# Kernel tuning notes

Measured on AMD Instinct MI355X. Metric: run time of the kernel, lower is better.

The kernel has to match this reference:

```python
import jax, jax.numpy as jnp
import numpy as np

EMBED_DIM = 1024
NUM_HEADS = 16
FFN_DIM = 4096
N_QUBITS = 8
LN_EPS = 1e-5


def _layernorm(x, g, b):
    mu = jnp.mean(x, axis=-1, keepdims=True)
    var = jnp.mean(jnp.square(x - mu), axis=-1, keepdims=True)
    return (x - mu) * jax.lax.rsqrt(var + LN_EPS) * g + b


def setup_inputs() -> dict:
    key = jax.random.key(0)
    ks = jax.random.split(key, 12)
    E, F_, Q = EMBED_DIM, FFN_DIM, N_QUBITS
    s = 1.0 / np.sqrt(E)
    return {
        "x": jax.random.normal(ks[0], (4, 2048, E), dtype=jnp.float32),
        "wq": jax.random.normal(ks[1], (E, E), dtype=jnp.float32) * s,
        "wk": jax.random.normal(ks[2], (E, E), dtype=jnp.float32) * s,
        "wv": jax.random.normal(ks[3], (E, E), dtype=jnp.float32) * s,
        "wo": jax.random.normal(ks[4], (E, E), dtype=jnp.float32) * s,
        "theta": jax.random.normal(ks[5], (Q,), dtype=jnp.float32),
        "w1": jax.random.normal(ks[6], (Q, F_), dtype=jnp.float32) * (1.0 / np.sqrt(Q)),
        "w2": jax.random.normal(ks[7], (F_, E), dtype=jnp.float32) * (1.0 / np.sqrt(F_)),
        "ln1_g": jnp.ones((E,), dtype=jnp.float32),
        "ln1_b": jnp.zeros((E,), dtype=jnp.float32),
        "ln2_g": jnp.ones((E,), dtype=jnp.float32),
        "ln2_b": jnp.zeros((E,), dtype=jnp.float32),
    }


def reference(x, wq, wk, wv, wo, theta, w1, w2, ln1_g, ln1_b, ln2_g, ln2_b):
    B, S, E = x.shape
    H, Dk = NUM_HEADS, E // NUM_HEADS
    # ---- multi-head attention ----
    q = (x @ wq).reshape(B, S, H, Dk).transpose(0, 2, 1, 3)  # [B,H,S,Dk]
    k = (x @ wk).reshape(B, S, H, Dk).transpose(0, 2, 1, 3)
    v = (x @ wv).reshape(B, S, H, Dk).transpose(0, 2, 1, 3)
    scores = jnp.einsum("bhsd,bhtd->bhst", q, k) / np.sqrt(Dk)
    attn = jax.nn.softmax(scores, axis=-1)
    ctx = jnp.einsum("bhst,bhtd->bhsd", attn, v)
    ctx = ctx.transpose(0, 2, 1, 3).reshape(B, S, E)
    attn_out = ctx @ wo
    x1 = _layernorm(x + attn_out, ln1_g, ln1_b)
    # ---- quantum FFN ----
    # Per qubit w: |0> -> RX(x1_w) -> RX(x1_w) -> RX(theta_w); <Z> = cos(2*x1_w + theta_w)
    q_out = jnp.cos(2.0 * x1[..., :N_QUBITS] + theta)  # [B,S,Q]
    ffn_out = jax.nn.relu(q_out @ w1) @ w2  # [B,S,E]
    return _layernorm(x1 + ffn_out, ln2_g, ln2_b)
```

## Files before the change

kernel.cpp:

```cpp
#include <hip/hip_runtime.h>
#include <hip/hip_bf16.h>


typedef __attribute__((ext_vector_type(8))) short bf16x8;
typedef __attribute__((ext_vector_type(16))) float f32x16;
typedef __attribute__((ext_vector_type(4))) unsigned short u16x4;

__device__ __forceinline__ unsigned short f2bf(float f) {
  union { float f; unsigned int u; } v; v.f = f;
  return (unsigned short)((v.u + 0x7FFFu + ((v.u >> 16) & 1u)) >> 16);
}
__device__ __forceinline__ float bf2f(unsigned short h) {
  union { unsigned int u; float f; } v; v.u = ((unsigned int)h) << 16;
  return v.f;
}
__device__ __forceinline__ f32x16 mfma32(bf16x8 a, bf16x8 b, f32x16 c) {
  return __builtin_amdgcn_mfma_f32_32x32x16_bf16(a, b, c, 0, 0, 0);
}
__device__ __forceinline__ void lds_cp16(const void* g, void* l) {
  __builtin_amdgcn_global_load_lds(
      (const __attribute__((address_space(1))) unsigned int*)g,
      (__attribute__((address_space(3))) unsigned int*)l, 16, 0, 0);
}

#define QG_CONV(P, FC0, FC1)                                                  \
  {                                                                           \
    int x0a, x0b, x1a, x1b, x2a, x2b, x3a, x3b;                               \
    asm("v_cvt_pk_bf16_f32 %0, %1, %2" : "=v"(x0a) : "v"(P[0]),  "v"(P[1]));  \
    asm("v_cvt_pk_bf16_f32 %0, %1, %2" : "=v"(x0b) : "v"(P[2]),  "v"(P[3]));  \
    asm("v_cvt_pk_bf16_f32 %0, %1, %2" : "=v"(x1a) : "v"(P[4]),  "v"(P[5]));  \
    asm("v_cvt_pk_bf16_f32 %0, %1, %2" : "=v"(x1b) : "v"(P[6]),  "v"(P[7]));  \
    asm("v_cvt_pk_bf16_f32 %0, %1, %2" : "=v"(x2a) : "v"(P[8]),  "v"(P[9]));  \
    asm("v_cvt_pk_bf16_f32 %0, %1, %2" : "=v"(x2b) : "v"(P[10]), "v"(P[11])); \
    asm("v_cvt_pk_bf16_f32 %0, %1, %2" : "=v"(x3a) : "v"(P[12]), "v"(P[13])); \
    asm("v_cvt_pk_bf16_f32 %0, %1, %2" : "=v"(x3b) : "v"(P[14]), "v"(P[15])); \
    asm("v_permlane32_swap_b32 %0, %1" : "+v"(x0a), "+v"(x1a));               \
    asm("v_permlane32_swap_b32 %0, %1" : "+v"(x0b), "+v"(x1b));               \
    asm("v_permlane32_swap_b32 %0, %1" : "+v"(x2a), "+v"(x3a));               \
    asm("v_permlane32_swap_b32 %0, %1" : "+v"(x2b), "+v"(x3b));               \
    union { int u[4]; bf16x8 v; } f0_, f1_;                                   \
    f0_.u[0] = x0a; f0_.u[1] = x0b; f0_.u[2] = x1a; f0_.u[3] = x1b;           \
    f1_.u[0] = x2a; f1_.u[1] = x2b; f1_.u[2] = x3a; f1_.u[3] = x3b;           \
    FC0 = f0_.v; FC1 = f1_.v;                                                 \
  }

__global__ __launch_bounds__(256) void cast_x_kernel(const float* __restrict__ in,
                                                     unsigned short* __restrict__ out,
                                                     int n4) {
  int i = blockIdx.x * 256 + threadIdx.x;
  if (i >= n4) return;
  float4 v = ((const float4*)in)[i];
  u16x4 o = { f2bf(v.x), f2bf(v.y), f2bf(v.z), f2bf(v.w) };
  ((u16x4*)out)[i] = o;
}

__global__ __launch_bounds__(256) void transpose_cast_kernel(const float* __restrict__ in,
                                                             unsigned short* __restrict__ out,
                                                             int K, int N) {
  __shared__ float tile[32][33];
  const int n0 = blockIdx.x * 32, k0 = blockIdx.y * 32;
  const int tx = threadIdx.x, ty = threadIdx.y;
#pragma unroll
  for (int i = 0; i < 32; i += 8)
    tile[ty + i][tx] = in[(long)(k0 + ty + i) * N + n0 + tx];
  __syncthreads();
#pragma unroll
  for (int i = 0; i < 32; i += 8)
    out[(long)(n0 + ty + i) * K + k0 + tx] = f2bf(tile[tx][ty + i]);
}

__global__ __launch_bounds__(256) void w1t_kernel(const float* __restrict__ w1,
                                                  unsigned short* __restrict__ w1t) {
  const int f = blockIdx.x * 256 + threadIdx.x;
  unsigned short v[8];
#pragma unroll
  for (int q = 0; q < 8; q++) v[q] = f2bf(w1[q * 4096 + f]);
  *(u16x4*)(w1t + f * 8)     = (u16x4){v[0], v[1], v[2], v[3]};
  *(u16x4*)(w1t + f * 8 + 4) = (u16x4){v[4], v[5], v[6], v[7]};
}

__global__ __launch_bounds__(256) void vt_kernel(const unsigned short* __restrict__ qkv,
                                                 unsigned short* __restrict__ vT) {
  __shared__ unsigned short tile[32][34];
  const int t0 = blockIdx.x * 32, d0 = blockIdx.y * 32, bh = blockIdx.z;
  const int b = bh >> 4, h = bh & 15;
  const int tx = threadIdx.x, ty = threadIdx.y;
  const unsigned short* src = qkv + (long)(b * 2048 + t0) * 3072 + 2048 + h * 64 + d0;
#pragma unroll
  for (int i = 0; i < 32; i += 8)
    tile[ty + i][tx] = src[(long)(ty + i) * 3072 + tx];
  __syncthreads();
  unsigned short* dst = vT + ((long)bh * 64 + d0) * 2048 + t0;
#pragma unroll
  for (int i = 0; i < 32; i += 8)
    dst[(long)(ty + i) * 2048 + tx] = tile[tx][ty + i];
}

template<int EPI>
__global__ __launch_bounds__(512) void gemm_bt2(const unsigned short* __restrict__ A,
                                                const unsigned short* __restrict__ BT,
                                                void* __restrict__ Cv,
                                                int M, int N, int K) {
  __shared__ __align__(16) unsigned char smem[2][49152];
  const int tid = threadIdx.x;
  const int l = tid & 63, w = tid >> 6;
  const int l32 = l & 31, h32 = l >> 5;
  const int wrm = (w >> 1) * 64;
  const int wrn = (w & 1) * 64;

  const int nx = gridDim.x;
  const int nwg = nx * gridDim.y;
  const int orig = blockIdx.y * nx + blockIdx.x;
  const int chunk = nwg >> 3;
  const int logical = (orig & 7) * chunk + (orig >> 3);
  const long m0 = (long)(logical / nx) * 256;
  const long n0 = (long)(logical % nx) * 128;

  const unsigned short* gp[6];
  unsigned ldsoff[6];
#pragma unroll
  for (int i = 0; i < 6; i++) {
    if (i < 4) {
      const int c = i * 512 + w * 64 + l;
      const int r = c >> 3, k8 = c & 7;
      gp[i] = A + (m0 + r) * (long)K + (k8 ^ (r & 7)) * 8;
    } else {
      const int c = (i - 4) * 512 + w * 64 + l;
      const int r = c >> 3, k8 = c & 7;
      gp[i] = BT + (n0 + r) * (long)K + (k8 ^ (r & 7)) * 8;
    }
    ldsoff[i] = (unsigned)(i * 512 + w * 64) * 16;
  }

  f32x16 acc[2][2];
#pragma unroll
  for (int mf = 0; mf < 2; mf++)
#pragma unroll
    for (int nf = 0; nf < 2; nf++)
#pragma unroll
      for (int e = 0; e < 16; e++) acc[mf][nf][e] = 0.f;

  const int NT = K >> 6;
#define STAGE(bf, t)                                                    \
  do {                                                                  \
    unsigned char* _d = &smem[bf][0];                                   \
    const long _ko = (long)(t) * 64;                                    \
    _Pragma("unroll")                                                   \
    for (int _i = 0; _i < 6; _i++)                                      \
      lds_cp16(gp[_i] + _ko, _d + ldsoff[_i]);                          \
  } while (0)

  STAGE(0, 0);
  int cur = 0;
  for (int t = 0; t < NT; t++) {
    if (t + 1 < NT) {
      STAGE(cur ^ 1, t + 1);
      asm volatile("s_waitcnt vmcnt(6)" ::: "memory");
    } else {
      asm volatile("s_waitcnt vmcnt(0)" ::: "memory");
    }
    __builtin_amdgcn_sched_barrier(0);
    __builtin_amdgcn_s_barrier();
    __builtin_amdgcn_sched_barrier(0);

    const unsigned char* bufA = &smem[cur][0];
    const unsigned char* bufB = &smem[cur][32768];
    bf16x8 af[2][4], bfr[2][4];
#pragma unroll
    for (int mf = 0; mf < 2; mf++) {
      const int r = wrm + mf * 32 + l32;
#pragma unroll
      for (int ks = 0; ks < 4; ks++)
        af[mf][ks] = *(const bf16x8*)(bufA + r * 128 + (((ks * 2 + h32) ^ (r & 7)) * 16));
    }
#pragma unroll
    for (int nf = 0; nf < 2; nf++) {
      const int r = wrn + nf * 32 + l32;
#pragma unroll
      for (int ks = 0; ks < 4; ks++)
        bfr[nf][ks] = *(const bf16x8*)(bufB + r * 128 + (((ks * 2 + h32) ^ (r & 7)) * 16));
    }
    __builtin_amdgcn_s_setprio(1);
#pragma unroll
    for (int ks = 0; ks < 4; ks++)
#pragma unroll
      for (int mf = 0; mf < 2; mf++)
#pragma unroll
        for (int nf = 0; nf < 2; nf++)
          acc[mf][nf] = mfma32(af[mf][ks], bfr[nf][ks], acc[mf][nf]);
    __builtin_amdgcn_s_setprio(0);
    __builtin_amdgcn_sched_barrier(0);
    __builtin_amdgcn_s_barrier();
    cur ^= 1;
  }
#undef STAGE

#pragma unroll
  for (int mf = 0; mf < 2; mf++)
#pragma unroll
    for (int nf = 0; nf < 2; nf++) {
      const long c0 = n0 + wrn + nf * 32 + l32;
#pragma unroll
      for (int reg = 0; reg < 16; reg++) {
        const long r0 = m0 + wrm + mf * 32 + (reg & 3) + 8 * (reg >> 2) + 4 * h32;
        if (EPI == 0) ((float*)Cv)[r0 * (long)N + c0] = acc[mf][nf][reg];
        else ((unsigned short*)Cv)[r0 * (long)N + c0] = f2bf(acc[mf][nf][reg]);
      }
    }
}

__global__ __launch_bounds__(512) void ffn_fused(const unsigned short* __restrict__ qo,
                                                 const unsigned short* __restrict__ w1t,
                                                 const unsigned short* __restrict__ BT,
                                                 float* __restrict__ C,
                                                 int N, int K) {
  __shared__ __align__(16) unsigned char sm[2 * 16384 + 65536 + 4096];
  unsigned char* lsW = sm + 32768;
  unsigned char* lsQ = sm + 98304;
  const int tid = threadIdx.x;
  const int l = tid & 63, w = tid >> 6;
  const int l32 = l & 31, h32 = l >> 5;
  const int wrm = (w >> 1) * 64;
  const int wrn = (w & 1) * 64;

  const int nx = gridDim.x;
  const int nwg = nx * gridDim.y;
  const int orig = blockIdx.y * nx + blockIdx.x;
  const int chunk = nwg >> 3;
  const int logical = (orig & 7) * chunk + (orig >> 3);
  const long m0 = (long)(logical / nx) * 256;
  const long n0 = (long)(logical % nx) * 128;

  const unsigned short* gpB[2];
  unsigned offB[2];
#pragma unroll
  for (int i = 0; i < 2; i++) {
    const int c = i * 512 + w * 64 + l;
    const int r = c >> 3, k8 = c & 7;
    gpB[i] = BT + (n0 + r) * (long)K + (k8 ^ (r & 7)) * 8;
    offB[i] = (unsigned)(i * 512 + w * 64) * 16;
  }

#pragma unroll
  for (int j = 0; j < 8; j++)
    lds_cp16(w1t + (long)(j * 512 + w * 64 + l) * 8, lsW + (unsigned)(j * 512 + w * 64) * 16);
  if (w < 4)
    lds_cp16(qo + (m0 + w * 64 + l) * 8, lsQ + (unsigned)(w * 64) * 16);
  lds_cp16(gpB[0], sm + offB[0]);
  lds_cp16(gpB[1], sm + offB[1]);
  asm volatile("s_waitcnt vmcnt(0)" ::: "memory");
  __builtin_amdgcn_s_barrier();

  const bf16x8 z8 = {0, 0, 0, 0, 0, 0, 0, 0};
  bf16x8 qof[2];
#pragma unroll
  for (int mf = 0; mf < 2; mf++)
    qof[mf] = (h32 == 0) ? *(const bf16x8*)(lsQ + (wrm + mf * 32 + l32) * 16) : z8;

  f32x16 zz;
#pragma unroll
  for (int e = 0; e < 16; e++) zz[e] = 0.f;
  f32x16 acc[2][2];
#pragma unroll
  for (int mf = 0; mf < 2; mf++)
#pragma unroll
    for (int nf = 0; nf < 2; nf++) acc[mf][nf] = zz;

  const int NT = K >> 6;
  int cur = 0;
  for (int t = 0; t < NT; t++) {
    if (t + 1 < NT) {
      unsigned char* d = sm + (cur ^ 1) * 16384;
      lds_cp16(gpB[0] + (long)(t + 1) * 64, d + offB[0]);
      lds_cp16(gpB[1] + (long)(t + 1) * 64, d + offB[1]);
      asm volatile("s_waitcnt vmcnt(2)" ::: "memory");
    } else {
      asm volatile("s_waitcnt vmcnt(0)" ::: "memory");
    }
    __builtin_amdgcn_sched_barrier(0);
    __builtin_amdgcn_s_barrier();
    __builtin_amdgcn_sched_barrier(0);

    bf16x8 w1f[2];
#pragma unroll
    for (int tg = 0; tg < 2; tg++)
      w1f[tg] = (h32 == 0) ? *(const bf16x8*)(lsW + (unsigned)(t * 64 + tg * 32 + l32) * 16) : z8;

    const unsigned char* bufB = sm + cur * 16384;
    bf16x8 bfr[2][4];
#pragma unroll
    for (int nf = 0; nf < 2; nf++) {
      const int r = wrn + nf * 32 + l32;
#pragma unroll
      for (int ks = 0; ks < 4; ks++)
        bfr[nf][ks] = *(const bf16x8*)(bufB + r * 128 + (((ks * 2 + h32) ^ (r & 7)) * 16));
    }

#pragma unroll
    for (int mf = 0; mf < 2; mf++) {
      __builtin_amdgcn_s_setprio(1);
      f32x16 hC0 = mfma32(w1f[0], qof[mf], zz);
      f32x16 hC1 = mfma32(w1f[1], qof[mf], zz);
      __builtin_amdgcn_s_setprio(0);
#pragma unroll
      for (int e = 0; e < 16; e++) {
        hC0[e] = fmaxf(hC0[e], 0.f);
        hC1[e] = fmaxf(hC1[e], 0.f);
      }
      bf16x8 a0, a1, a2, a3;
      QG_CONV(hC0, a0, a1)
      QG_CONV(hC1, a2, a3)
      __builtin_amdgcn_s_setprio(1);
      acc[mf][0] = mfma32(a0, bfr[0][0], acc[mf][0]);
      acc[mf][0] = mfma32(a1, bfr[0][1], acc[mf][0]);
      acc[mf][0] = mfma32(a2, bfr[0][2], acc[mf][0]);
      acc[mf][0] = mfma32(a3, bfr[0][3], acc[mf][0]);
      acc[mf][1] = mfma32(a0, bfr[1][0], acc[mf][1]);
      acc[mf][1] = mfma32(a1, bfr[1][1], acc[mf][1]);
      acc[mf][1] = mfma32(a2, bfr[1][2], acc[mf][1]);
      acc[mf][1] = mfma32(a3, bfr[1][3], acc[mf][1]);
      __builtin_amdgcn_s_setprio(0);
    }
    __builtin_amdgcn_sched_barrier(0);
    __builtin_amdgcn_s_barrier();
    cur ^= 1;
  }

#pragma unroll
  for (int mf = 0; mf < 2; mf++)
#pragma unroll
    for (int nf = 0; nf < 2; nf++) {
      const long c0 = n0 + wrn + nf * 32 + l32;
#pragma unroll
      for (int reg = 0; reg < 16; reg++) {
        const long r0 = m0 + wrm + mf * 32 + (reg & 3) + 8 * (reg >> 2) + 4 * h32;
        C[r0 * (long)N + c0] = acc[mf][nf][reg];
      }
    }
}

#define QG_BLOCK(P, LIP, FC0, FC1)                                            \
  {                                                                           \
    _Pragma("unroll")                                                         \
    for (int e = 0; e < 16; e++)                                              \
      asm("v_exp_f32 %0, %1" : "=v"(P[e]) : "v"(P[e]));                       \
    float s_ = 0.f;                                                           \
    _Pragma("unroll")                                                         \
    for (int e = 0; e < 16; e++) s_ += P[e];                                  \
    LIP += s_;                                                                \
    QG_CONV(P, FC0, FC1)                                                      \
  }

__global__ __launch_bounds__(256) void attn_kernel(const unsigned short* __restrict__ qkv,
                                                   const unsigned short* __restrict__ vT,
                                                   unsigned short* __restrict__ ctx) {
  __shared__ __align__(16) unsigned short lsK[64][72];
  __shared__ __align__(16) unsigned short lsV[64][72];

  const int tid = threadIdx.x;
  const int l = tid & 63, w = tid >> 6;
  const int l32 = l & 31, h32 = l >> 5;

  const int orig = blockIdx.x;
  const int logical = (orig & 7) * 64 + (orig >> 3);
  const int s0 = (logical & 7) * 256;
  const int bh = logical >> 3;
  const int b = bh >> 4, hh = bh & 15;

  const float QSC = 0.18033688f;
  const unsigned short* qg_base = qkv + (long)(b * 2048 + s0 + w * 64) * 3072 + hh * 64;
  bf16x8 qb0[4], qb1[4];
#pragma unroll
  for (int kc = 0; kc < 4; kc++) {
    bf16x8 t0v = *(const bf16x8*)(qg_base + (long)l32 * 3072 + kc * 16 + h32 * 8);
    bf16x8 t1v = *(const bf16x8*)(qg_base + (long)(32 + l32) * 3072 + kc * 16 + h32 * 8);
#pragma unroll
    for (int j = 0; j < 8; j++) {
      t0v[j] = (short)f2bf(bf2f((unsigned short)t0v[j]) * QSC);
      t1v[j] = (short)f2bf(bf2f((unsigned short)t1v[j]) * QSC);
    }
    qb0[kc] = t0v;
    qb1[kc] = t1v;
  }

  f32x16 oacc00, oacc01, oacc10, oacc11;
#pragma unroll
  for (int e = 0; e < 16; e++) {
    oacc00[e] = 0.f; oacc01[e] = 0.f; oacc10[e] = 0.f; oacc11[e] = 0.f;
  }
  float lip0 = 0.f, lip1 = 0.f;

  const int tr = tid >> 2;
  const int tc = (tid & 3) * 16;
  const unsigned short* kbase = qkv + (long)(b * 2048) * 3072 + 1024 + hh * 64;
  const unsigned short* vbase = vT + (long)bh * 64 * 2048;

  bf16x8 k0 = *(const bf16x8*)(kbase + (long)tr * 3072 + tc);
  bf16x8 k1 = *(const bf16x8*)(kbase + (long)tr * 3072 + tc + 8);
  bf16x8 v0 = *(const bf16x8*)(vbase + (long)tr * 2048 + tc);
  bf16x8 v1 = *(const bf16x8*)(vbase + (long)tr * 2048 + tc + 8);

  for (int t0 = 0; t0 < 2048; t0 += 64) {
    __syncthreads();
    *(bf16x8*)&lsK[tr][tc]     = k0;
    *(bf16x8*)&lsK[tr][tc + 8] = k1;
    *(bf16x8*)&lsV[tr][tc]     = v0;
    *(bf16x8*)&lsV[tr][tc + 8] = v1;
    __syncthreads();
    if (t0 + 64 < 2048) {
      k0 = *(const bf16x8*)(kbase + (long)(t0 + 64 + tr) * 3072 + tc);
      k1 = *(const bf16x8*)(kbase + (long)(t0 + 64 + tr) * 3072 + tc + 8);
      v0 = *(const bf16x8*)(vbase + (long)tr * 2048 + t0 + 64 + tc);
      v1 = *(const bf16x8*)(vbase + (long)tr * 2048 + t0 + 64 + tc + 8);
    }

#pragma unroll
    for (int tg = 0; tg < 2; tg++) {
      bf16x8 kb[4];
#pragma unroll
      for (int kc = 0; kc < 4; kc++)
        kb[kc] = *(const bf16x8*)&lsK[tg * 32 + l32][kc * 16 + h32 * 8];

      f32x16 p0, p1;
#pragma unroll
      for (int e = 0; e < 16; e++) { p0[e] = 0.f; p1[e] = 0.f; }
      __builtin_amdgcn_s_setprio(1);
#pragma unroll
      for (int kc = 0; kc < 4; kc++) {
        p0 = mfma32(kb[kc], qb0[kc], p0);
        p1 = mfma32(kb[kc], qb1[kc], p1);
      }
      __builtin_amdgcn_s_setprio(0);

      bf16x8 fA0, fA1, fB0, fB1;
      QG_BLOCK(p0, lip0, fA0, fA1)
      QG_BLOCK(p1, lip1, fB0, fB1)

      bf16x8 v00 = *(const bf16x8*)&lsV[l32][tg * 32 + h32 * 8];
      bf16x8 v01 = *(const bf16x8*)&lsV[l32][tg * 32 + 16 + h32 * 8];
      bf16x8 v10 = *(const bf16x8*)&lsV[32 + l32][tg * 32 + h32 * 8];
      bf16x8 v11 = *(const bf16x8*)&lsV[32 + l32][tg * 32 + 16 + h32 * 8];

      __builtin_amdgcn_s_setprio(1);
      oacc00 = mfma32(fA0, v00, oacc00);
      oacc00 = mfma32(fA1, v01, oacc00);
      oacc01 = mfma32(fA0, v10, oacc01);
      oacc01 = mfma32(fA1, v11, oacc01);
      oacc10 = mfma32(fB0, v00, oacc10);
      oacc10 = mfma32(fB1, v01, oacc10);
      oacc11 = mfma32(fB0, v10, oacc11);
      oacc11 = mfma32(fB1, v11, oacc11);
      __builtin_amdgcn_s_setprio(0);
    }
  }

  const float li0 = lip0 + __shfl_xor(lip0, 32);
  const float li1 = lip1 + __shfl_xor(lip1, 32);
  const float inv0 = 1.f / li0;
  const float inv1 = 1.f / li1;
  const long qrow0 = (long)(b * 2048 + s0 + w * 64);
  const int dcol = hh * 64 + l32;
#define STORE_QG(OA, OB, INV, QOFF)                                           \
  _Pragma("unroll")                                                           \
  for (int reg = 0; reg < 16; reg++) {                                        \
    const int rq = (reg & 3) + 8 * (reg >> 2) + 4 * h32;                      \
    const float iv = __shfl(INV, rq);                                         \
    const long q = qrow0 + (QOFF) + rq;                                       \
    ctx[q * 1024 + dcol]      = f2bf(OA[reg] * iv);                           \
    ctx[q * 1024 + dcol + 32] = f2bf(OB[reg] * iv);                           \
  }
  STORE_QG(oacc00, oacc01, inv0, 0)
  STORE_QG(oacc10, oacc11, inv1, 32)
#undef STORE_QG
}

template<bool QO>
__global__ __launch_bounds__(256) void ln_kernel(const float* __restrict__ ra,
                                                 const float* __restrict__ rb,
                                                 const float* __restrict__ g,
                                                 const float* __restrict__ bb,
                                                 float* __restrict__ out,
                                                 unsigned short* __restrict__ qo,
                                                 const float* __restrict__ theta) {
  const int row = blockIdx.x;
  const int tid = threadIdx.x;
  const long base = (long)row * 1024 + tid * 4;
  float4 a = *(const float4*)(ra + base);
  float4 bv = *(const float4*)(rb + base);
  float4 r;
  r.x = a.x + bv.x; r.y = a.y + bv.y; r.z = a.z + bv.z; r.w = a.w + bv.w;
  float s  = r.x + r.y + r.z + r.w;
  float ss = r.x * r.x + r.y * r.y + r.z * r.z + r.w * r.w;
  for (int off = 32; off; off >>= 1) {
    s  += __shfl_down(s, off);
    ss += __shfl_down(ss, off);
  }
  __shared__ float red[4][2];
  const int wv = tid >> 6;
  if ((tid & 63) == 0) { red[wv][0] = s; red[wv][1] = ss; }
  __syncthreads();
  s  = red[0][0] + red[1][0] + red[2][0] + red[3][0];
  ss = red[0][1] + red[1][1] + red[2][1] + red[3][1];
  const float mu  = s * (1.f / 1024.f);
  const float var = ss * (1.f / 1024.f) - mu * mu;
  const float rsv = rsqrtf(var + 1e-5f);
  float4 gv  = *(const float4*)(g + tid * 4);
  float4 bbv = *(const float4*)(bb + tid * 4);
  float4 y;
  y.x = (r.x - mu) * rsv * gv.x + bbv.x;
  y.y = (r.y - mu) * rsv * gv.y + bbv.y;
  y.z = (r.z - mu) * rsv * gv.z + bbv.z;
  y.w = (r.w - mu) * rsv * gv.w + bbv.w;
  *(float4*)(out + base) = y;
  if constexpr (QO) {
    if (tid < 2) {
      float yv[4] = {y.x, y.y, y.z, y.w};
      u16x4 o;
#pragma unroll
      for (int c = 0; c < 4; c++)
        o[c] = f2bf(__cosf(2.f * yv[c] + theta[tid * 4 + c]));
      *(u16x4*)(qo + (long)row * 8 + tid * 4) = o;
    }
  }
}

extern "C" void kernel_launch(void* const* d_in, const int* in_sizes, int n_in,
                              void* d_out, int out_size, void* d_ws, size_t ws_size,
                              hipStream_t stream) {
  const float* x     = (const float*)d_in[0];
  const float* wq    = (const float*)d_in[1];
  const float* wk    = (const float*)d_in[2];
  const float* wv    = (const float*)d_in[3];
  const float* wo    = (const float*)d_in[4];
  const float* theta = (const float*)d_in[5];
  const float* w1    = (const float*)d_in[6];
  const float* w2    = (const float*)d_in[7];
  const float* g1    = (const float*)d_in[8];
  const float* b1    = (const float*)d_in[9];
  const float* g2    = (const float*)d_in[10];
  const float* b2    = (const float*)d_in[11];
  float* out = (float*)d_out;
  char* ws = (char*)d_ws;

  const long MB = 1 << 20;
  unsigned short* xb    = (unsigned short*)(ws);
  unsigned short* wqkvT = (unsigned short*)(ws + 16 * MB);
  unsigned short* woT   = (unsigned short*)(ws + 22 * MB);
  unsigned short* w2T   = (unsigned short*)(ws + 24 * MB);
  float*          x1    = (float*)(ws + 32 * MB);
  float*          fbuf  = (float*)(ws + 64 * MB);
  unsigned short* qkv   = (unsigned short*)(ws + 96 * MB);
  unsigned short* vTb   = (unsigned short*)(ws + 144 * MB);
  unsigned short* qob   = (unsigned short*)(ws + 160 * MB);
  unsigned short* w1tb  = (unsigned short*)(ws + 160 * MB + 128 * 1024);
  unsigned short* ctx   = xb;

  cast_x_kernel<<<8192, 256, 0, stream>>>(x, xb, 8192 * 1024 / 4);
  dim3 tb(32, 8);
  transpose_cast_kernel<<<dim3(32, 32), tb, 0, stream>>>(wq, wqkvT, 1024, 1024);
  transpose_cast_kernel<<<dim3(32, 32), tb, 0, stream>>>(wk, wqkvT + 1024 * 1024, 1024, 1024);
  transpose_cast_kernel<<<dim3(32, 32), tb, 0, stream>>>(wv, wqkvT + 2048 * 1024, 1024, 1024);
  transpose_cast_kernel<<<dim3(32, 32), tb, 0, stream>>>(wo, woT, 1024, 1024);
  transpose_cast_kernel<<<dim3(32, 128), tb, 0, stream>>>(w2, w2T, 4096, 1024);
  w1t_kernel<<<16, 256, 0, stream>>>(w1, w1tb);

  gemm_bt2<1><<<dim3(24, 32), 512, 0, stream>>>(xb, wqkvT, qkv, 8192, 3072, 1024);

  vt_kernel<<<dim3(64, 2, 64), tb, 0, stream>>>(qkv, vTb);

  attn_kernel<<<512, 256, 0, stream>>>(qkv, vTb, ctx);

  gemm_bt2<0><<<dim3(8, 32), 512, 0, stream>>>(ctx, woT, fbuf, 8192, 1024, 1024);

  ln_kernel<true><<<8192, 256, 0, stream>>>(x, fbuf, g1, b1, x1, qob, theta);

  ffn_fused<<<dim3(8, 32), 512, 0, stream>>>(qob, w1tb, w2T, fbuf, 1024, 4096);

  ln_kernel<false><<<8192, 256, 0, stream>>>(x1, fbuf, g2, b2, out, nullptr, nullptr);
}
```

Baseline: 338.7 us.

## Shrink GEMM and FFN tiles to 128x128 with 256-thread blocks

Both the QKV/output-projection GEMM and the fused FFN kernel move from 256x128 tiles with 512 threads to 128x128 tiles with 256 threads. Grids double and LDS use per block drops, so more blocks can be resident and the work spreads more evenly over the CUs. The FFN kernel also stops staging the whole w1 table in LDS; it prefetches the w1 fragments for the next k-step straight from global memory into registers alongside the B tile load. In exchange, each block gets less operand reuse, so there is more global and L2 traffic per flop.

```diff
diff --git a/kernel.cpp b/kernel.cpp
--- a/kernel.cpp
+++ b/kernel.cpp
@@ -97,11 +97,11 @@
 }
 
 template<int EPI>
-__global__ __launch_bounds__(512) void gemm_bt2(const unsigned short* __restrict__ A,
+__global__ __launch_bounds__(256) void gemm_bt3(const unsigned short* __restrict__ A,
                                                 const unsigned short* __restrict__ BT,
                                                 void* __restrict__ Cv,
                                                 int M, int N, int K) {
-  __shared__ __align__(16) unsigned char smem[2][49152];
+  __shared__ __align__(16) unsigned char smem[2][32768];
   const int tid = threadIdx.x;
   const int l = tid & 63, w = tid >> 6;
   const int l32 = l & 31, h32 = l >> 5;
@@ -113,23 +113,22 @@
   const int orig = blockIdx.y * nx + blockIdx.x;
   const int chunk = nwg >> 3;
   const int logical = (orig & 7) * chunk + (orig >> 3);
-  const long m0 = (long)(logical / nx) * 256;
+  const long m0 = (long)(logical / nx) * 128;
   const long n0 = (long)(logical % nx) * 128;
 
-  const unsigned short* gp[6];
-  unsigned ldsoff[6];
-#pragma unroll
-  for (int i = 0; i < 6; i++) {
+  const unsigned short* gp[8];
+  unsigned ldsoff[8];
+#pragma unroll
+  for (int i = 0; i < 8; i++) {
+    const int c = (i & 3) * 256 + tid;
+    const int r = c >> 3, k8 = c & 7;
     if (i < 4) {
-      const int c = i * 512 + w * 64 + l;
-      const int r = c >> 3, k8 = c & 7;
       gp[i] = A + (m0 + r) * (long)K + (k8 ^ (r & 7)) * 8;
+      ldsoff[i] = (unsigned)c * 16;
     } else {
-      const int c = (i - 4) * 512 + w * 64 + l;
-      const int r = c >> 3, k8 = c & 7;
       gp[i] = BT + (n0 + r) * (long)K + (k8 ^ (r & 7)) * 8;
-    }
-    ldsoff[i] = (unsigned)(i * 512 + w * 64) * 16;
+      ldsoff[i] = 16384u + (unsigned)c * 16;
+    }
   }
 
   f32x16 acc[2][2];
@@ -146,7 +145,7 @@
     unsigned char* _d = &smem[bf][0];                                   \
     const long _ko = (long)(t) * 64;                                    \
     _Pragma("unroll")                                                   \
-    for (int _i = 0; _i < 6; _i++)                                      \
+    for (int _i = 0; _i < 8; _i++)                                      \
       lds_cp16(gp[_i] + _ko, _d + ldsoff[_i]);                          \
   } while (0)
 
@@ -155,7 +154,7 @@
   for (int t = 0; t < NT; t++) {
     if (t + 1 < NT) {
       STAGE(cur ^ 1, t + 1);
-      asm volatile("s_waitcnt vmcnt(6)" ::: "memory");
+      asm volatile("s_waitcnt vmcnt(8)" ::: "memory");
     } else {
       asm volatile("s_waitcnt vmcnt(0)" ::: "memory");
     }
@@ -164,7 +163,7 @@
     __builtin_amdgcn_sched_barrier(0);
 
     const unsigned char* bufA = &smem[cur][0];
-    const unsigned char* bufB = &smem[cur][32768];
+    const unsigned char* bufB = &smem[cur][16384];
     bf16x8 af[2][4], bfr[2][4];
 #pragma unroll
     for (int mf = 0; mf < 2; mf++) {
@@ -209,14 +208,13 @@
     }
 }
 
-__global__ __launch_bounds__(512) void ffn_fused(const unsigned short* __restrict__ qo,
+__global__ __launch_bounds__(256) void ffn_fused(const unsigned short* __restrict__ qo,
                                                  const unsigned short* __restrict__ w1t,
                                                  const unsigned short* __restrict__ BT,
                                                  float* __restrict__ C,
                                                  int N, int K) {
-  __shared__ __align__(16) unsigned char sm[2 * 16384 + 65536 + 4096];
-  unsigned char* lsW = sm + 32768;
-  unsigned char* lsQ = sm + 98304;
+  __shared__ __align__(16) unsigned char sm[2 * 16384 + 2048];
+  unsigned char* lsQ = sm + 32768;
   const int tid = threadIdx.x;
   const int l = tid & 63, w = tid >> 6;
   const int l32 = l & 31, h32 = l >> 5;
@@ -228,30 +226,40 @@
   const int orig = blockIdx.y * nx + blockIdx.x;
   const int chunk = nwg >> 3;
   const int logical = (orig & 7) * chunk + (orig >> 3);
-  const long m0 = (long)(logical / nx) * 256;
+  const long m0 = (long)(logical / nx) * 128;
   const long n0 = (long)(logical % nx) * 128;
 
-  const unsigned short* gpB[2];
-  unsigned offB[2];
-#pragma unroll
-  for (int i = 0; i < 2; i++) {
-    const int c = i * 512 + w * 64 + l;
+  const unsigned short* gpB[4];
+  unsigned offB[4];
+#pragma unroll
+  for (int i = 0; i < 4; i++) {
+    const int c = i * 256 + tid;
     const int r = c >> 3, k8 = c & 7;
     gpB[i] = BT + (n0 + r) * (long)K + (k8 ^ (r & 7)) * 8;
-    offB[i] = (unsigned)(i * 512 + w * 64) * 16;
-  }
-
-#pragma unroll
-  for (int j = 0; j < 8; j++)
-    lds_cp16(w1t + (long)(j * 512 + w * 64 + l) * 8, lsW + (unsigned)(j * 512 + w * 64) * 16);
-  if (w < 4)
-    lds_cp16(qo + (m0 + w * 64 + l) * 8, lsQ + (unsigned)(w * 64) * 16);
-  lds_cp16(gpB[0], sm + offB[0]);
-  lds_cp16(gpB[1], sm + offB[1]);
+    offB[i] = (unsigned)c * 16;
+  }
+
+  const bf16x8 z8 = {0, 0, 0, 0, 0, 0, 0, 0};
+  const int NT = K >> 6;
+
+#define STAGE_B(bf, t)                                                  \
+  do {                                                                  \
+    unsigned char* _d = sm + (bf) * 16384;                              \
+    const long _ko = (long)(t) * 64;                                    \
+    _Pragma("unroll")                                                   \
+    for (int _i = 0; _i < 4; _i++)                                      \
+      lds_cp16(gpB[_i] + _ko, _d + offB[_i]);                           \
+  } while (0)
+
+  STAGE_B(0, 0);
+  if (w < 2) lds_cp16(qo + (m0 + w * 64 + l) * 8, lsQ + (unsigned)(w * 64) * 16);
+  bf16x8 w1cur[2], w1nxt[2];
+#pragma unroll
+  for (int tg = 0; tg < 2; tg++)
+    w1cur[tg] = (h32 == 0) ? *(const bf16x8*)(w1t + (long)(tg * 32 + l32) * 8) : z8;
   asm volatile("s_waitcnt vmcnt(0)" ::: "memory");
   __builtin_amdgcn_s_barrier();
 
-  const bf16x8 z8 = {0, 0, 0, 0, 0, 0, 0, 0};
   bf16x8 qof[2];
 #pragma unroll
   for (int mf = 0; mf < 2; mf++)
@@ -266,14 +274,15 @@
 #pragma unroll
     for (int nf = 0; nf < 2; nf++) acc[mf][nf] = zz;
 
-  const int NT = K >> 6;
   int cur = 0;
   for (int t = 0; t < NT; t++) {
     if (t + 1 < NT) {
-      unsigned char* d = sm + (cur ^ 1) * 16384;
-      lds_cp16(gpB[0] + (long)(t + 1) * 64, d + offB[0]);
-      lds_cp16(gpB[1] + (long)(t + 1) * 64, d + offB[1]);
-      asm volatile("s_waitcnt vmcnt(2)" ::: "memory");
+      STAGE_B(cur ^ 1, t + 1);
+#pragma unroll
+      for (int tg = 0; tg < 2; tg++)
+        w1nxt[tg] = (h32 == 0)
+            ? *(const bf16x8*)(w1t + (long)((t + 1) * 64 + tg * 32 + l32) * 8) : z8;
+      asm volatile("s_waitcnt vmcnt(6)" ::: "memory");
     } else {
       asm volatile("s_waitcnt vmcnt(0)" ::: "memory");
     }
@@ -281,11 +290,6 @@
     __builtin_amdgcn_s_barrier();
     __builtin_amdgcn_sched_barrier(0);
 
-    bf16x8 w1f[2];
-#pragma unroll
-    for (int tg = 0; tg < 2; tg++)
-      w1f[tg] = (h32 == 0) ? *(const bf16x8*)(lsW + (unsigned)(t * 64 + tg * 32 + l32) * 16) : z8;
-
     const unsigned char* bufB = sm + cur * 16384;
     bf16x8 bfr[2][4];
 #pragma unroll
@@ -299,8 +303,8 @@
 #pragma unroll
     for (int mf = 0; mf < 2; mf++) {
       __builtin_amdgcn_s_setprio(1);
-      f32x16 hC0 = mfma32(w1f[0], qof[mf], zz);
-      f32x16 hC1 = mfma32(w1f[1], qof[mf], zz);
+      f32x16 hC0 = mfma32(w1cur[0], qof[mf], zz);
+      f32x16 hC1 = mfma32(w1cur[1], qof[mf], zz);
       __builtin_amdgcn_s_setprio(0);
 #pragma unroll
       for (int e = 0; e < 16; e++) {
@@ -323,8 +327,11 @@
     }
     __builtin_amdgcn_sched_barrier(0);
     __builtin_amdgcn_s_barrier();
+    w1cur[0] = w1nxt[0];
+    w1cur[1] = w1nxt[1];
     cur ^= 1;
   }
+#undef STAGE_B
 
 #pragma unroll
   for (int mf = 0; mf < 2; mf++)
@@ -564,17 +571,17 @@
   transpose_cast_kernel<<<dim3(32, 128), tb, 0, stream>>>(w2, w2T, 4096, 1024);
   w1t_kernel<<<16, 256, 0, stream>>>(w1, w1tb);
 
-  gemm_bt2<1><<<dim3(24, 32), 512, 0, stream>>>(xb, wqkvT, qkv, 8192, 3072, 1024);
+  gemm_bt3<1><<<dim3(24, 64), 256, 0, stream>>>(xb, wqkvT, qkv, 8192, 3072, 1024);
 
   vt_kernel<<<dim3(64, 2, 64), tb, 0, stream>>>(qkv, vTb);
 
   attn_kernel<<<512, 256, 0, stream>>>(qkv, vTb, ctx);
 
-  gemm_bt2<0><<<dim3(8, 32), 512, 0, stream>>>(ctx, woT, fbuf, 8192, 1024, 1024);
+  gemm_bt3<0><<<dim3(8, 64), 256, 0, stream>>>(ctx, woT, fbuf, 8192, 1024, 1024);
 
   ln_kernel<true><<<8192, 256, 0, stream>>>(x, fbuf, g1, b1, x1, qob, theta);
 
-  ffn_fused<<<dim3(8, 32), 512, 0, stream>>>(qob, w1tb, w2T, fbuf, 1024, 4096);
+  ffn_fused<<<dim3(8, 64), 256, 0, stream>>>(qob, w1tb, w2T, fbuf, 1024, 4096);
 
   ln_kernel<false><<<8192, 256, 0, stream>>>(x1, fbuf, g2, b2, out, nullptr, nullptr);
 }
```

After: 365.4 us. +7.9%, slower.
